# Kernel optimization log

Measured on AMD Instinct MI355X. Metric: run time of the kernel, lower is better.

The kernel has to match this reference:

```python
import jax, jax.numpy as jnp
import numpy as np

BS, SEQ, D, H = 2, 2048, 1024, 16
HD = D // H  # head_dim = 64


def setup_inputs() -> dict:
    key = jax.random.key(0)
    kx, kw = jax.random.split(key)
    x = jax.random.normal(kx, (BS, SEQ, D), dtype=jnp.float32)
    # qkv Linear: weight [3D, D] (xavier_normal), bias zeros
    std = float(np.sqrt(2.0 / (D + 3 * D)))
    W_qkv = jax.random.normal(kw, (3 * D, D), dtype=jnp.float32) * std
    b_qkv = jnp.zeros((3 * D,), dtype=jnp.float32)
    return {"x": x, "W_qkv": W_qkv, "b_qkv": b_qkv}


def reference(x, W_qkv, b_qkv):
    bs, seq_len, embed_dim = x.shape
    # fused QKV projection: [bs, seq, 3D]
    qkv = x @ W_qkv.T + b_qkv
    qkv = qkv.reshape(bs, seq_len, 3, H, HD)
    qkv = jnp.transpose(qkv, (2, 0, 3, 1, 4))  # [3, bs, H, seq, HD]
    Q, K, V = qkv[0], qkv[1], qkv[2]
    # past_kv is None -> total_len == seq_len, past_len == 0
    scores = jnp.einsum("bhqd,bhkd->bhqk", Q, K) / jnp.sqrt(jnp.float32(HD))
    # causal mask: True above diagonal -> -inf
    mask = jnp.triu(jnp.ones((seq_len, seq_len), dtype=bool), k=1)
    scores = jnp.where(mask[None, None, :, :], -jnp.inf, scores)
    probs = jax.nn.softmax(scores, axis=-1)
    # attn_dropout = 0.0 (eval) -> identity
    out = jnp.einsum("bhqk,bhkd->bhqd", probs, V)
    out = jnp.transpose(out, (0, 2, 1, 3)).reshape(bs, seq_len, embed_dim)
    return (out, (K, V))
```

## Files before the change

kernel.cpp:

```cpp
#include <hip/hip_runtime.h>

typedef __bf16 bf16_t;
typedef __bf16 bf16x8 __attribute__((ext_vector_type(8)));
typedef float f32x4 __attribute__((ext_vector_type(4)));

__device__ __forceinline__ bf16_t f2bf(float f) {
  unsigned u = __float_as_uint(f);
  u += 0x7fffu + ((u >> 16) & 1u);
  unsigned short s = (unsigned short)(u >> 16);
  union { unsigned short s; bf16_t b; } cv; cv.s = s; return cv.b;
}

__device__ __forceinline__ void gl16(const void* g, void* l) {
  __builtin_amdgcn_global_load_lds(
      (const __attribute__((address_space(1))) void*)g,
      (__attribute__((address_space(3))) void*)l,
      16, 0, 0);
}

__global__ __launch_bounds__(256) void cvt_kernel(const float* __restrict__ src,
                                                  bf16_t* __restrict__ dst, int n8) {
  int i = blockIdx.x * 256 + threadIdx.x;
  if (i >= n8) return;
  const float4* s = (const float4*)src + (size_t)i * 2;
  float4 a = s[0], b = s[1];
  bf16x8 o;
  o[0] = f2bf(a.x); o[1] = f2bf(a.y); o[2] = f2bf(a.z); o[3] = f2bf(a.w);
  o[4] = f2bf(b.x); o[5] = f2bf(b.y); o[6] = f2bf(b.z); o[7] = f2bf(b.w);
  const int row = i >> 7, jr = i & 127;
  const int g = jr >> 2, jj = jr & 3;
  const int dstc = (row << 7) + (g << 2) + (jj ^ ((row >> 1) & 3));
  *((bf16x8*)dst + dstc) = o;
}

#define GEMM_K 1024
__global__ __launch_bounds__(256) void qkv_gemm(
    const bf16_t* __restrict__ A,
    const bf16_t* __restrict__ B,
    const float* __restrict__ bias,
    float* __restrict__ Ko, float* __restrict__ Vo,
    bf16_t* __restrict__ Qb, bf16_t* __restrict__ Kb,
    bf16_t* __restrict__ Vt)
{
  __shared__ bf16_t lsA[128 * 32];
  __shared__ bf16_t lsB[128 * 32];
  const int tid = threadIdx.x;
  const int lane = tid & 63;
  const int ln = lane & 15, qd = lane >> 4;
  const int wid = tid >> 6;
  const int wm = wid & 1, wn = wid >> 1;
  const int bm = blockIdx.x & 31, bn = blockIdx.x >> 5;
  const int m0 = bm * 128, n0 = bn * 128;
  const int qs = qd ^ ((ln >> 1) & 3);

  f32x4 acc[4][4] = {};

  const int c0 = tid, c1 = tid + 256;
  const bf16_t* ga0 = A + (size_t)(m0 + (c0 >> 2)) * GEMM_K + (c0 & 3) * 8;
  const bf16_t* ga1 = A + (size_t)(m0 + (c1 >> 2)) * GEMM_K + (c1 & 3) * 8;
  const bf16_t* gb0 = B + (size_t)(n0 + (c0 >> 2)) * GEMM_K + (c0 & 3) * 8;
  const bf16_t* gb1 = B + (size_t)(n0 + (c1 >> 2)) * GEMM_K + (c1 & 3) * 8;
  bf16_t* la0 = &lsA[c0 * 8];
  bf16_t* la1 = &lsA[c1 * 8];
  bf16_t* lb0 = &lsB[c0 * 8];
  bf16_t* lb1 = &lsB[c1 * 8];

  for (int k0 = 0; k0 < GEMM_K; k0 += 32) {
    __syncthreads();
    gl16(ga0 + k0, la0);
    gl16(ga1 + k0, la1);
    gl16(gb0 + k0, lb0);
    gl16(gb1 + k0, lb1);
    __syncthreads();
    bf16x8 af[4], bf[4];
#pragma unroll
    for (int mi = 0; mi < 4; ++mi)
      af[mi] = *(const bf16x8*)&lsA[(wm * 64 + mi * 16 + ln) * 32 + qs * 8];
#pragma unroll
    for (int ni = 0; ni < 4; ++ni)
      bf[ni] = *(const bf16x8*)&lsB[(wn * 64 + ni * 16 + ln) * 32 + qs * 8];
#pragma unroll
    for (int mi = 0; mi < 4; ++mi)
#pragma unroll
      for (int ni = 0; ni < 4; ++ni)
        acc[mi][ni] = __builtin_amdgcn_mfma_f32_16x16x32_bf16(af[mi], bf[ni], acc[mi][ni], 0, 0, 0);
  }

  const int sec = n0 >> 10;
#pragma unroll
  for (int mi = 0; mi < 4; ++mi) {
#pragma unroll
    for (int ni = 0; ni < 4; ++ni) {
      const int colg = n0 + wn * 64 + ni * 16 + ln;
      const float bv = bias[colg];
      const int cc = colg & 1023, h = cc >> 6, hd = cc & 63;
#pragma unroll
      for (int r = 0; r < 4; ++r) {
        const int mg = m0 + wm * 64 + mi * 16 + qd * 4 + r;
        const int b = mg >> 11, s = mg & 2047;
        const float val = acc[mi][ni][r] + bv;
        const int bhi = b * 16 + h;
        const size_t pidx = ((size_t)(bhi * 2048 + s)) * 64 + hd;
        const size_t sidx = (size_t)bhi * 131072 + (size_t)(s >> 6) * 4096 +
                            (size_t)(s & 63) * 64 + (((hd >> 3) ^ (s & 7)) << 3) + (hd & 7);
        if (sec == 0) {
          Qb[sidx] = f2bf(val);
        } else if (sec == 1) {
          Ko[pidx] = val;
          Kb[sidx] = f2bf(val);
        } else {
          Vo[pidx] = val;
          const size_t vidx = (size_t)bhi * 131072 + (size_t)(s >> 6) * 4096 +
                              (size_t)hd * 64 + ((((s >> 3) & 7) ^ (hd & 7)) << 3) + (s & 7);
          Vt[vidx] = f2bf(val);
        }
      }
    }
  }
}

#define LP_STRIDE 72
__global__ __launch_bounds__(256) void attn_kernel(
    const bf16_t* __restrict__ Qb,
    const bf16_t* __restrict__ Kb,
    const bf16_t* __restrict__ Vt,
    float* __restrict__ Out)
{
  __shared__ bf16_t lq[128 * 64];
  __shared__ bf16_t lk[64 * 64];
  __shared__ bf16_t lv[64 * 64];
  __shared__ bf16_t lp[128 * LP_STRIDE];
  const int tid = threadIdx.x;
  const int lane = tid & 63, ln = lane & 15, qd = lane >> 4;
  const int w = tid >> 6;

  const int bidx = blockIdx.x;
  const int bh = bidx & 31;
  const int x = bidx >> 5;
  const int it = (bidx < 256) ? (15 - x) : (x - 8);
  const int b = bh >> 4, h = bh & 15;

  const bf16_t* qbase = Qb + (size_t)bh * 131072 + (size_t)it * 8192;
  const bf16_t* kbase = Kb + (size_t)bh * 131072;
  const bf16_t* vbase = Vt + (size_t)bh * 131072;

#pragma unroll
  for (int i = 0; i < 4; ++i) {
    int cc = tid + i * 256;
    gl16(qbase + cc * 8, &lq[cc * 8]);
  }
  __syncthreads();
  bf16x8 afq[2][2];
#pragma unroll
  for (int kk = 0; kk < 2; ++kk)
#pragma unroll
    for (int mi = 0; mi < 2; ++mi) {
      const int row = w * 32 + mi * 16 + ln;
      afq[kk][mi] = *(const bf16x8*)&lq[(row >> 6) * 4096 + (row & 63) * 64 +
                                        (((kk * 4 + qd) ^ (ln & 7)) << 3)];
    }

  f32x4 oc[2][4] = {};
  float lsum[2][4] = {};
  const float C1 = 0.125f * 1.44269504f;

  const int jt1 = 2 * it + 2;
  for (int jt = 0; jt < jt1; ++jt) {
    __syncthreads();
    {
      const bf16_t* kt = kbase + (size_t)jt * 4096;
      const bf16_t* vt = vbase + (size_t)jt * 4096;
      int cc = tid, c2 = tid + 256;
      gl16(kt + cc * 8, &lk[cc * 8]);
      gl16(kt + c2 * 8, &lk[c2 * 8]);
      gl16(vt + cc * 8, &lv[cc * 8]);
      gl16(vt + c2 * 8, &lv[c2 * 8]);
    }
    __syncthreads();

    f32x4 sa[2][4] = {};
#pragma unroll
    for (int kk = 0; kk < 2; ++kk) {
      bf16x8 bfk[4];
#pragma unroll
      for (int ni = 0; ni < 4; ++ni)
        bfk[ni] = *(const bf16x8*)&lk[(ni * 16 + ln) * 64 + (((kk * 4 + qd) ^ (ln & 7)) << 3)];
#pragma unroll
      for (int mi = 0; mi < 2; ++mi)
#pragma unroll
        for (int ni = 0; ni < 4; ++ni)
          sa[mi][ni] = __builtin_amdgcn_mfma_f32_16x16x32_bf16(afq[kk][mi], bfk[ni], sa[mi][ni], 0, 0, 0);
    }

    const bool diag = (jt >= 2 * it);
#pragma unroll
    for (int mi = 0; mi < 2; ++mi) {
#pragma unroll
      for (int r = 0; r < 4; ++r) {
        const int rowg = it * 128 + w * 32 + mi * 16 + qd * 4 + r;
#pragma unroll
        for (int ni = 0; ni < 4; ++ni) {
          float sv = sa[mi][ni][r] * C1;
          if (diag) {
            int colg = jt * 64 + ni * 16 + ln;
            if (colg > rowg) sv = -10000.f;
          }
          float p = __builtin_amdgcn_exp2f(sv);
          sa[mi][ni][r] = p;
          lsum[mi][r] += p;
        }
      }
    }

#pragma unroll
    for (int mi = 0; mi < 2; ++mi)
#pragma unroll
      for (int ni = 0; ni < 4; ++ni)
#pragma unroll
        for (int r = 0; r < 4; ++r)
          lp[(w * 32 + mi * 16 + qd * 4 + r) * LP_STRIDE + ni * 16 + ln] = f2bf(sa[mi][ni][r]);

#pragma unroll
    for (int kk = 0; kk < 2; ++kk) {
      bf16x8 afp[2], bfv[4];
#pragma unroll
      for (int mi = 0; mi < 2; ++mi)
        afp[mi] = *(const bf16x8*)&lp[(w * 32 + mi * 16 + ln) * LP_STRIDE + kk * 32 + qd * 8];
#pragma unroll
      for (int ni = 0; ni < 4; ++ni)
        bfv[ni] = *(const bf16x8*)&lv[(ni * 16 + ln) * 64 + (((kk * 4 + qd) ^ (ln & 7)) << 3)];
#pragma unroll
      for (int mi = 0; mi < 2; ++mi)
#pragma unroll
        for (int ni = 0; ni < 4; ++ni)
          oc[mi][ni] = __builtin_amdgcn_mfma_f32_16x16x32_bf16(afp[mi], bfv[ni], oc[mi][ni], 0, 0, 0);
    }
  }

#pragma unroll
  for (int mi = 0; mi < 2; ++mi) {
#pragma unroll
    for (int r = 0; r < 4; ++r) {
      float ls = lsum[mi][r];
      ls += __shfl_xor(ls, 1);
      ls += __shfl_xor(ls, 2);
      ls += __shfl_xor(ls, 4);
      ls += __shfl_xor(ls, 8);
      const float inv = 1.0f / ls;
      const int rowq = it * 128 + w * 32 + mi * 16 + qd * 4 + r;
#pragma unroll
      for (int ni = 0; ni < 4; ++ni) {
        const int colh = ni * 16 + ln;
        Out[(size_t)(b * 2048 + rowq) * 1024 + h * 64 + colh] = oc[mi][ni][r] * inv;
      }
    }
  }
}

extern "C" void kernel_launch(void* const* d_in, const int* in_sizes, int n_in,
                              void* d_out, int out_size, void* d_ws, size_t ws_size,
                              hipStream_t stream) {
  const float* x = (const float*)d_in[0];
  const float* W = (const float*)d_in[1];
  const float* bq = (const float*)d_in[2];
  float* out = (float*)d_out;
  float* Ko = out + 4194304;
  float* Vo = out + 8388608;
  char* ws = (char*)d_ws;
  bf16_t* xb = (bf16_t*)ws;
  bf16_t* wb = (bf16_t*)(ws + 8388608);
  bf16_t* Qb = (bf16_t*)(ws + 14680064);
  bf16_t* Kb = (bf16_t*)(ws + 23068672);
  bf16_t* Vt = (bf16_t*)(ws + 31457280);

  hipLaunchKernelGGL(cvt_kernel, dim3(2048), dim3(256), 0, stream, x, xb, 524288);
  hipLaunchKernelGGL(cvt_kernel, dim3(1536), dim3(256), 0, stream, W, wb, 393216);
  hipLaunchKernelGGL(qkv_gemm, dim3(768), dim3(256), 0, stream, xb, wb, bq, Ko, Vo, Qb, Kb, Vt);
  hipLaunchKernelGGL(attn_kernel, dim3(512), dim3(256), 0, stream, Qb, Kb, Vt, out);
}
```

Baseline: 191.6 us.

## Persistent attention with atomic work queue, double-buffered K/V, transposed S, merged convert

The attention kernel becomes persistent, with 256 blocks pulling (query tile, head) tasks from an atomic counter that the GEMM kernel resets. K/V tiles are double-buffered so the next tile loads while the current one computes. The QK^T product is computed transposed so probabilities can be packed into 64-bit swizzled LDS stores, and row-sum reduction uses fewer shuffles. The two convert launches are merged into one. Risks are the atomic contention and the extra LDS use lowering occupancy.

```diff
diff --git a/kernel.cpp b/kernel.cpp
--- a/kernel.cpp
+++ b/kernel.cpp
@@ -4,10 +4,13 @@
 typedef __bf16 bf16x8 __attribute__((ext_vector_type(8)));
 typedef float f32x4 __attribute__((ext_vector_type(4)));
 
-__device__ __forceinline__ bf16_t f2bf(float f) {
+__device__ __forceinline__ unsigned short bfbits(float f) {
   unsigned u = __float_as_uint(f);
   u += 0x7fffu + ((u >> 16) & 1u);
-  unsigned short s = (unsigned short)(u >> 16);
+  return (unsigned short)(u >> 16);
+}
+__device__ __forceinline__ bf16_t f2bf(float f) {
+  unsigned short s = bfbits(f);
   union { unsigned short s; bf16_t b; } cv; cv.s = s; return cv.b;
 }
 
@@ -18,18 +21,21 @@
       16, 0, 0);
 }
 
-__global__ __launch_bounds__(256) void cvt_kernel(const float* __restrict__ src,
-                                                  bf16_t* __restrict__ dst, int n8) {
-  int i = blockIdx.x * 256 + threadIdx.x;
-  if (i >= n8) return;
-  const float4* s = (const float4*)src + (size_t)i * 2;
+__global__ __launch_bounds__(256) void cvt_kernel(const float* __restrict__ x,
+                                                  const float* __restrict__ Wf,
+                                                  bf16_t* __restrict__ xb,
+                                                  bf16_t* __restrict__ wb) {
+  const int i = blockIdx.x * 256 + threadIdx.x;
+  const float* src; bf16_t* dst; int j;
+  if (i < 524288) { j = i; src = x; dst = xb; }
+  else            { j = i - 524288; src = Wf; dst = wb; }
+  const float4* s = (const float4*)src + (size_t)j * 2;
   float4 a = s[0], b = s[1];
   bf16x8 o;
   o[0] = f2bf(a.x); o[1] = f2bf(a.y); o[2] = f2bf(a.z); o[3] = f2bf(a.w);
   o[4] = f2bf(b.x); o[5] = f2bf(b.y); o[6] = f2bf(b.z); o[7] = f2bf(b.w);
-  const int row = i >> 7, jr = i & 127;
-  const int g = jr >> 2, jj = jr & 3;
-  const int dstc = (row << 7) + (g << 2) + (jj ^ ((row >> 1) & 3));
+  const int row = j >> 7, jr = j & 127;
+  const int dstc = (row << 7) + (jr & ~3) + ((jr & 3) ^ ((row >> 1) & 3));
   *((bf16x8*)dst + dstc) = o;
 }
 
@@ -40,8 +46,10 @@
     const float* __restrict__ bias,
     float* __restrict__ Ko, float* __restrict__ Vo,
     bf16_t* __restrict__ Qb, bf16_t* __restrict__ Kb,
-    bf16_t* __restrict__ Vt)
+    bf16_t* __restrict__ Vt,
+    int* __restrict__ qcnt)
 {
+  if (blockIdx.x == 0 && threadIdx.x == 0) *qcnt = 0;
   __shared__ bf16_t lsA[128 * 32];
   __shared__ bf16_t lsB[128 * 32];
   const int tid = threadIdx.x;
@@ -119,139 +127,153 @@
   }
 }
 
-#define LP_STRIDE 72
 __global__ __launch_bounds__(256) void attn_kernel(
     const bf16_t* __restrict__ Qb,
     const bf16_t* __restrict__ Kb,
     const bf16_t* __restrict__ Vt,
-    float* __restrict__ Out)
+    float* __restrict__ Out,
+    int* __restrict__ qcnt)
 {
   __shared__ bf16_t lq[128 * 64];
-  __shared__ bf16_t lk[64 * 64];
-  __shared__ bf16_t lv[64 * 64];
-  __shared__ bf16_t lp[128 * LP_STRIDE];
+  __shared__ bf16_t lk[2][64 * 64];
+  __shared__ bf16_t lv[2][64 * 64];
+  __shared__ bf16_t lp[128 * 64];
+  __shared__ int task_sh;
   const int tid = threadIdx.x;
   const int lane = tid & 63, ln = lane & 15, qd = lane >> 4;
   const int w = tid >> 6;
-
-  const int bidx = blockIdx.x;
-  const int bh = bidx & 31;
-  const int x = bidx >> 5;
-  const int it = (bidx < 256) ? (15 - x) : (x - 8);
-  const int b = bh >> 4, h = bh & 15;
-
-  const bf16_t* qbase = Qb + (size_t)bh * 131072 + (size_t)it * 8192;
-  const bf16_t* kbase = Kb + (size_t)bh * 131072;
-  const bf16_t* vbase = Vt + (size_t)bh * 131072;
-
-#pragma unroll
-  for (int i = 0; i < 4; ++i) {
-    int cc = tid + i * 256;
-    gl16(qbase + cc * 8, &lq[cc * 8]);
-  }
-  __syncthreads();
-  bf16x8 afq[2][2];
-#pragma unroll
-  for (int kk = 0; kk < 2; ++kk)
-#pragma unroll
-    for (int mi = 0; mi < 2; ++mi) {
-      const int row = w * 32 + mi * 16 + ln;
-      afq[kk][mi] = *(const bf16x8*)&lq[(row >> 6) * 4096 + (row & 63) * 64 +
-                                        (((kk * 4 + qd) ^ (ln & 7)) << 3)];
-    }
-
-  f32x4 oc[2][4] = {};
-  float lsum[2][4] = {};
+  const int l7 = ln & 7;
   const float C1 = 0.125f * 1.44269504f;
 
-  const int jt1 = 2 * it + 2;
-  for (int jt = 0; jt < jt1; ++jt) {
-    __syncthreads();
+  for (;;) {
+    __syncthreads();
+    if (tid == 0) task_sh = atomicAdd(qcnt, 1);
+    __syncthreads();
+    const int task = task_sh;
+    if (task >= 512) break;
+    const int it = 15 - (task >> 5);
+    const int bh = task & 31;
+    const int b = bh >> 4, h = bh & 15;
+    const int jt1 = 2 * it + 2;
+
+    const bf16_t* qbase = Qb + (size_t)bh * 131072 + (size_t)it * 8192;
+    const bf16_t* kbase = Kb + (size_t)bh * 131072;
+    const bf16_t* vbase = Vt + (size_t)bh * 131072;
+
+#pragma unroll
+    for (int i = 0; i < 4; ++i) { const int cc = tid + i * 256; gl16(qbase + cc * 8, &lq[cc * 8]); }
     {
-      const bf16_t* kt = kbase + (size_t)jt * 4096;
-      const bf16_t* vt = vbase + (size_t)jt * 4096;
-      int cc = tid, c2 = tid + 256;
-      gl16(kt + cc * 8, &lk[cc * 8]);
-      gl16(kt + c2 * 8, &lk[c2 * 8]);
-      gl16(vt + cc * 8, &lv[cc * 8]);
-      gl16(vt + c2 * 8, &lv[c2 * 8]);
-    }
-    __syncthreads();
-
-    f32x4 sa[2][4] = {};
-#pragma unroll
-    for (int kk = 0; kk < 2; ++kk) {
-      bf16x8 bfk[4];
-#pragma unroll
-      for (int ni = 0; ni < 4; ++ni)
-        bfk[ni] = *(const bf16x8*)&lk[(ni * 16 + ln) * 64 + (((kk * 4 + qd) ^ (ln & 7)) << 3)];
-#pragma unroll
-      for (int mi = 0; mi < 2; ++mi)
+      const int cc = tid, c2 = tid + 256;
+      gl16(kbase + cc * 8, &lk[0][cc * 8]);
+      gl16(kbase + c2 * 8, &lk[0][c2 * 8]);
+      gl16(vbase + cc * 8, &lv[0][cc * 8]);
+      gl16(vbase + c2 * 8, &lv[0][c2 * 8]);
+    }
+    __syncthreads();
+
+    bf16x8 afq[2][2];
+#pragma unroll
+    for (int kk = 0; kk < 2; ++kk)
+#pragma unroll
+      for (int qi = 0; qi < 2; ++qi) {
+        const int row = w * 32 + qi * 16 + ln;
+        afq[kk][qi] = *(const bf16x8*)&lq[(row >> 6) * 4096 + (row & 63) * 64 +
+                                          (((kk * 4 + qd) ^ l7) << 3)];
+      }
+
+    f32x4 oc[2][4] = {};
+    float lsum[2] = {0.f, 0.f};
+    const int qg = it * 128 + w * 32 + ln;
+
+    for (int jt = 0; jt < jt1; ++jt) {
+      if (jt > 0) __syncthreads();
+      const int cur = jt & 1;
+      if (jt + 1 < jt1) {
+        const bf16_t* kt = kbase + (size_t)(jt + 1) * 4096;
+        const bf16_t* vt = vbase + (size_t)(jt + 1) * 4096;
+        const int nxt = cur ^ 1;
+        const int cc = tid, c2 = tid + 256;
+        gl16(kt + cc * 8, &lk[nxt][cc * 8]);
+        gl16(kt + c2 * 8, &lk[nxt][c2 * 8]);
+        gl16(vt + cc * 8, &lv[nxt][cc * 8]);
+        gl16(vt + c2 * 8, &lv[nxt][c2 * 8]);
+      }
+
+      f32x4 sa[4][2] = {};
+#pragma unroll
+      for (int kk = 0; kk < 2; ++kk) {
+        bf16x8 ak[4];
+#pragma unroll
+        for (int ki = 0; ki < 4; ++ki)
+          ak[ki] = *(const bf16x8*)&lk[cur][(ki * 16 + ln) * 64 + (((kk * 4 + qd) ^ l7) << 3)];
+#pragma unroll
+        for (int ki = 0; ki < 4; ++ki)
+#pragma unroll
+          for (int qi = 0; qi < 2; ++qi)
+            sa[ki][qi] = __builtin_amdgcn_mfma_f32_16x16x32_bf16(ak[ki], afq[kk][qi], sa[ki][qi], 0, 0, 0);
+      }
+
+      const bool diag = (jt >= 2 * it);
+#pragma unroll
+      for (int qi = 0; qi < 2; ++qi) {
+        const int qgl = qg + qi * 16;
+        const int q = w * 32 + qi * 16 + ln;
+#pragma unroll
+        for (int ki = 0; ki < 4; ++ki) {
+          const int kb0 = jt * 64 + ki * 16 + qd * 4;
+          unsigned long long pk = 0;
+#pragma unroll
+          for (int r = 0; r < 4; ++r) {
+            float sv = sa[ki][qi][r] * C1;
+            if (diag && (kb0 + r > qgl)) sv = -10000.f;
+            const float p = __builtin_amdgcn_exp2f(sv);
+            lsum[qi] += p;
+            pk |= ((unsigned long long)bfbits(p)) << (16 * r);
+          }
+          const int g = (ki * 2 + (qd >> 1)) ^ l7;
+          *(unsigned long long*)&lp[q * 64 + g * 8 + (qd & 1) * 4] = pk;
+        }
+      }
+
+#pragma unroll
+      for (int kk = 0; kk < 2; ++kk) {
+        bf16x8 afp[2], bfv[4];
+#pragma unroll
+        for (int qi = 0; qi < 2; ++qi) {
+          const int q = w * 32 + qi * 16 + ln;
+          afp[qi] = *(const bf16x8*)&lp[q * 64 + (((kk * 4 + qd) ^ l7) << 3)];
+        }
 #pragma unroll
         for (int ni = 0; ni < 4; ++ni)
-          sa[mi][ni] = __builtin_amdgcn_mfma_f32_16x16x32_bf16(afq[kk][mi], bfk[ni], sa[mi][ni], 0, 0, 0);
-    }
-
-    const bool diag = (jt >= 2 * it);
-#pragma unroll
-    for (int mi = 0; mi < 2; ++mi) {
+          bfv[ni] = *(const bf16x8*)&lv[cur][(ni * 16 + ln) * 64 + (((kk * 4 + qd) ^ l7) << 3)];
+#pragma unroll
+        for (int qi = 0; qi < 2; ++qi)
+#pragma unroll
+          for (int ni = 0; ni < 4; ++ni)
+            oc[qi][ni] = __builtin_amdgcn_mfma_f32_16x16x32_bf16(afp[qi], bfv[ni], oc[qi][ni], 0, 0, 0);
+      }
+    }
+
+    float lsq[2];
+#pragma unroll
+    for (int qi = 0; qi < 2; ++qi) {
+      float ls = lsum[qi];
+      ls += __shfl_xor(ls, 16);
+      ls += __shfl_xor(ls, 32);
+      lsq[qi] = ls;
+    }
+#pragma unroll
+    for (int qi = 0; qi < 2; ++qi) {
 #pragma unroll
       for (int r = 0; r < 4; ++r) {
-        const int rowg = it * 128 + w * 32 + mi * 16 + qd * 4 + r;
+        const float lval = __shfl(lsq[qi], qd * 4 + r);
+        const float inv = 1.0f / lval;
+        const int rowq = it * 128 + w * 32 + qi * 16 + qd * 4 + r;
 #pragma unroll
         for (int ni = 0; ni < 4; ++ni) {
-          float sv = sa[mi][ni][r] * C1;
-          if (diag) {
-            int colg = jt * 64 + ni * 16 + ln;
-            if (colg > rowg) sv = -10000.f;
-          }
-          float p = __builtin_amdgcn_exp2f(sv);
-          sa[mi][ni][r] = p;
-          lsum[mi][r] += p;
+          const int colh = ni * 16 + ln;
+          Out[(size_t)(b * 2048 + rowq) * 1024 + h * 64 + colh] = oc[qi][ni][r] * inv;
         }
-      }
-    }
-
-#pragma unroll
-    for (int mi = 0; mi < 2; ++mi)
-#pragma unroll
-      for (int ni = 0; ni < 4; ++ni)
-#pragma unroll
-        for (int r = 0; r < 4; ++r)
-          lp[(w * 32 + mi * 16 + qd * 4 + r) * LP_STRIDE + ni * 16 + ln] = f2bf(sa[mi][ni][r]);
-
-#pragma unroll
-    for (int kk = 0; kk < 2; ++kk) {
-      bf16x8 afp[2], bfv[4];
-#pragma unroll
-      for (int mi = 0; mi < 2; ++mi)
-        afp[mi] = *(const bf16x8*)&lp[(w * 32 + mi * 16 + ln) * LP_STRIDE + kk * 32 + qd * 8];
-#pragma unroll
-      for (int ni = 0; ni < 4; ++ni)
-        bfv[ni] = *(const bf16x8*)&lv[(ni * 16 + ln) * 64 + (((kk * 4 + qd) ^ (ln & 7)) << 3)];
-#pragma unroll
-      for (int mi = 0; mi < 2; ++mi)
-#pragma unroll
-        for (int ni = 0; ni < 4; ++ni)
-          oc[mi][ni] = __builtin_amdgcn_mfma_f32_16x16x32_bf16(afp[mi], bfv[ni], oc[mi][ni], 0, 0, 0);
-    }
-  }
-
-#pragma unroll
-  for (int mi = 0; mi < 2; ++mi) {
-#pragma unroll
-    for (int r = 0; r < 4; ++r) {
-      float ls = lsum[mi][r];
-      ls += __shfl_xor(ls, 1);
-      ls += __shfl_xor(ls, 2);
-      ls += __shfl_xor(ls, 4);
-      ls += __shfl_xor(ls, 8);
-      const float inv = 1.0f / ls;
-      const int rowq = it * 128 + w * 32 + mi * 16 + qd * 4 + r;
-#pragma unroll
-      for (int ni = 0; ni < 4; ++ni) {
-        const int colh = ni * 16 + ln;
-        Out[(size_t)(b * 2048 + rowq) * 1024 + h * 64 + colh] = oc[mi][ni][r] * inv;
       }
     }
   }
@@ -272,9 +294,9 @@
   bf16_t* Qb = (bf16_t*)(ws + 14680064);
   bf16_t* Kb = (bf16_t*)(ws + 23068672);
   bf16_t* Vt = (bf16_t*)(ws + 31457280);
-
-  hipLaunchKernelGGL(cvt_kernel, dim3(2048), dim3(256), 0, stream, x, xb, 524288);
-  hipLaunchKernelGGL(cvt_kernel, dim3(1536), dim3(256), 0, stream, W, wb, 393216);
-  hipLaunchKernelGGL(qkv_gemm, dim3(768), dim3(256), 0, stream, xb, wb, bq, Ko, Vo, Qb, Kb, Vt);
-  hipLaunchKernelGGL(attn_kernel, dim3(512), dim3(256), 0, stream, Qb, Kb, Vt, out);
-}
+  int*    qcnt = (int*)(ws + 39845888);
+
+  hipLaunchKernelGGL(cvt_kernel, dim3(3584), dim3(256), 0, stream, x, W, xb, wb);
+  hipLaunchKernelGGL(qkv_gemm, dim3(768), dim3(256), 0, stream, xb, wb, bq, Ko, Vo, Qb, Kb, Vt, qcnt);
+  hipLaunchKernelGGL(attn_kernel, dim3(256), dim3(256), 0, stream, Qb, Kb, Vt, out, qcnt);
+}
```

New measurement: 192.0 us. About the same (+0.2%).
